# Optimization experiments

Measured on AMD Instinct MI355X. Metric: run time of the kernel, lower is better.

## Reference

```python
import jax, jax.numpy as jnp
import numpy as np
from jax import lax

B, T_HIST, T_PRED = 8192, 11, 80
IN, H = 2, 64


def _glorot(key, shape, fan):
    bound = 1.0 / np.sqrt(fan)
    return jax.random.uniform(key, shape, jnp.float32, -bound, bound)


def setup_inputs() -> dict:
    key = jax.random.key(0)
    ks = jax.random.split(key, 20)
    inp = {"x": jax.random.normal(ks[0], (B, T_HIST, IN), jnp.float32)}
    # encoder / decoder: 2-layer tanh RNN, PyTorch param layout (out_features first)
    for pfx, base in (("enc", 1), ("dec", 9)):
        inp[f"{pfx}_Wih0"] = _glorot(ks[base + 0], (H, IN), H)
        inp[f"{pfx}_Whh0"] = _glorot(ks[base + 1], (H, H), H)
        inp[f"{pfx}_bih0"] = _glorot(ks[base + 2], (H,), H)
        inp[f"{pfx}_bhh0"] = _glorot(ks[base + 3], (H,), H)
        inp[f"{pfx}_Wih1"] = _glorot(ks[base + 4], (H, H), H)
        inp[f"{pfx}_Whh1"] = _glorot(ks[base + 5], (H, H), H)
        inp[f"{pfx}_bih1"] = _glorot(ks[base + 6], (H,), H)
        inp[f"{pfx}_bhh1"] = _glorot(ks[base + 7], (H,), H)
    inp["fc_W"] = _glorot(ks[17], (2, H), H)
    inp["fc_b"] = _glorot(ks[18], (2,), H)
    return inp


def _rnn_layer(x_seq, h0, Wih, Whh, bih, bhh):
    # x_seq: [T, B, in]; tanh RNN cell, returns (h_T, all hidden states [T, B, H])
    def step(h, x_t):
        h_new = jnp.tanh(x_t @ Wih.T + bih + h @ Whh.T + bhh)
        return h_new, h_new
    return lax.scan(step, h0, x_seq)


def reference(x,
              enc_Wih0, enc_Whh0, enc_bih0, enc_bhh0,
              enc_Wih1, enc_Whh1, enc_bih1, enc_bhh1,
              dec_Wih0, dec_Whh0, dec_bih0, dec_bhh0,
              dec_Wih1, dec_Whh1, dec_bih1, dec_bhh1,
              fc_W, fc_b):
    b = x.shape[0]
    h0 = jnp.zeros((b, H), x.dtype)
    x_seq = jnp.swapaxes(x, 0, 1)  # [T, B, 2]
    # encoder (dropout inactive in eval)
    h1_T, hs0 = _rnn_layer(x_seq, h0, enc_Wih0, enc_Whh0, enc_bih0, enc_bhh0)
    h2_T, _ = _rnn_layer(hs0, h0, enc_Wih1, enc_Whh1, enc_bih1, enc_bhh1)

    def dec_step(carry, _):
        h1, h2, inp = carry
        h1 = jnp.tanh(inp @ dec_Wih0.T + dec_bih0 + h1 @ dec_Whh0.T + dec_bhh0)
        h2 = jnp.tanh(h1 @ dec_Wih1.T + dec_bih1 + h2 @ dec_Whh1.T + dec_bhh1)
        pred = h2 @ fc_W.T + fc_b  # [B, 2]
        return (h1, h2, pred), pred

    init = (h1_T, h2_T, x[:, -1, :])
    _, preds = lax.scan(dec_step, init, None, length=T_PRED)  # [80, B, 2]
    return jnp.swapaxes(preds, 0, 1)  # [B, 80, 2]
```

## Files before the change

kernel.cpp:

```cpp
#include <hip/hip_runtime.h>

typedef __attribute__((ext_vector_type(8))) __bf16 bf16x8;
typedef __attribute__((ext_vector_type(4))) float  f32x4;

namespace {
constexpr int kB    = 8192;
constexpr int kTH   = 11;
constexpr int kTP   = 80;
constexpr int kM    = 16;
constexpr int kStrH = 72;
}

union FragU { bf16x8 v; unsigned u[4]; };

__device__ __forceinline__ bf16x8 zero_frag() {
    FragU z; z.u[0] = z.u[1] = z.u[2] = z.u[3] = 0u; return z.v;
}

__device__ __forceinline__ unsigned pack_hi16(unsigned a, unsigned b) {
    return (a >> 16) | (b & 0xFFFF0000u);
}

__device__ __forceinline__ void split8(const float* f, bf16x8& hi, bf16x8& lo) {
    FragU H, L;
#pragma unroll
    for (int w = 0; w < 4; ++w) {
        const unsigned u0 = __float_as_uint(f[2 * w + 0]);
        const unsigned u1 = __float_as_uint(f[2 * w + 1]);
        const float h0 = __uint_as_float(u0 & 0xFFFF0000u);
        const float h1 = __uint_as_float(u1 & 0xFFFF0000u);
        const unsigned l0 = __float_as_uint(f[2 * w + 0] - h0);
        const unsigned l1 = __float_as_uint(f[2 * w + 1] - h1);
        H.u[w] = pack_hi16(u0, u1);
        L.u[w] = pack_hi16(l0, l1);
    }
    hi = H.v; lo = L.v;
}

__device__ __forceinline__ void loadB1(const float* __restrict__ W, int col, int q,
                                       bf16x8 (&Bh)[2], bf16x8 (&Bl)[2]) {
#pragma unroll
    for (int c = 0; c < 2; ++c) {
        const float* src = W + col * 64 + c * 32 + q * 8;
        const float4 a = reinterpret_cast<const float4*>(src)[0];
        const float4 b = reinterpret_cast<const float4*>(src)[1];
        float f[8] = {a.x, a.y, a.z, a.w, b.x, b.y, b.z, b.w};
        split8(f, Bh[c], Bl[c]);
    }
}

__device__ __forceinline__ void loadBfc(const float* __restrict__ fcW, int p, int q,
                                        bf16x8 (&Bh)[2], bf16x8 (&Bl)[2]) {
#pragma unroll
    for (int c = 0; c < 2; ++c) {
        float f[8];
#pragma unroll
        for (int j = 0; j < 8; ++j)
            f[j] = (p < 2) ? fcW[p * 64 + c * 32 + q * 8 + j] : 0.f;
        split8(f, Bh[c], Bl[c]);
    }
}

__device__ __forceinline__ void loadBG(const float* __restrict__ fcW, float w0, float w1,
                                       int q, bf16x8 (&Bh)[2], bf16x8 (&Bl)[2]) {
#pragma unroll
    for (int c = 0; c < 2; ++c) {
        float f[8];
#pragma unroll
        for (int j = 0; j < 8; ++j) {
            const int k = c * 32 + q * 8 + j;
            f[j] = w0 * fcW[k] + w1 * fcW[64 + k];
        }
        split8(f, Bh[c], Bl[c]);
    }
}

__device__ __forceinline__ void write_h(unsigned short* hi, unsigned short* lo,
                                        int idx, float h) {
    const unsigned u = __float_as_uint(h);
    hi[idx] = (unsigned short)(u >> 16);
    const float hf = __uint_as_float(u & 0xFFFF0000u);
    const float l  = h - hf;
    lo[idx] = (unsigned short)(__float_as_uint(l) >> 16);
}

__device__ __forceinline__ bf16x8 read_frag(const unsigned short* plane, int off) {
    return *reinterpret_cast<const bf16x8*>(plane + off);
}

__device__ __forceinline__ f32x4 mfma3(bf16x8 ah, bf16x8 al, bf16x8 bh, bf16x8 bl, f32x4 acc) {
    acc = __builtin_amdgcn_mfma_f32_16x16x32_bf16(ah, bh, acc, 0, 0, 0);
    acc = __builtin_amdgcn_mfma_f32_16x16x32_bf16(ah, bl, acc, 0, 0, 0);
    acc = __builtin_amdgcn_mfma_f32_16x16x32_bf16(al, bh, acc, 0, 0, 0);
    return acc;
}

__device__ __forceinline__ float fast_tanh(float x) {
    const float e = __builtin_amdgcn_exp2f(x * 2.8853900817779268f);
    return fmaf(-2.0f, __builtin_amdgcn_rcpf(e + 1.0f), 1.0f);
}

__global__ __attribute__((amdgpu_waves_per_eu(2, 2))) __launch_bounds__(256)
void traj_rnn_kernel(
    const float* __restrict__ x,
    const float* __restrict__ eWih0, const float* __restrict__ eWhh0,
    const float* __restrict__ ebih0, const float* __restrict__ ebhh0,
    const float* __restrict__ eWih1, const float* __restrict__ eWhh1,
    const float* __restrict__ ebih1, const float* __restrict__ ebhh1,
    const float* __restrict__ dWih0, const float* __restrict__ dWhh0,
    const float* __restrict__ dbih0, const float* __restrict__ dbhh0,
    const float* __restrict__ dWih1, const float* __restrict__ dWhh1,
    const float* __restrict__ dbih1, const float* __restrict__ dbhh1,
    const float* __restrict__ fcW, const float* __restrict__ fcb,
    float* __restrict__ out)
{
    const int tid  = threadIdx.x;
    const int wv   = tid >> 6;
    const int lane = tid & 63;
    const int p    = lane & 15;
    const int q    = lane >> 4;
    const int col  = wv * 16 + p;
    const int r0   = blockIdx.x * kM;

    __shared__ __align__(16) unsigned short Hhi1[kM * kStrH], Hlo1[kM * kStrH];
    __shared__ __align__(16) unsigned short Hhi2[kM * kStrH], Hlo2[kM * kStrH];
    __shared__ __align__(16) float xbuf[kM * kTH * 2];

    for (int i = tid; i < kM * kTH * 2; i += 256)
        xbuf[i] = x[r0 * (kTH * 2) + i];

    bf16x8 H1h[2], H1l[2], H2h[2], H2l[2];
#pragma unroll
    for (int c = 0; c < 2; ++c) {
        H1h[c] = zero_frag(); H1l[c] = zero_frag();
        H2h[c] = zero_frag(); H2l[c] = zero_frag();
    }
    __syncthreads();

    const int aoff = p * kStrH;

    {
        const float b0 = ebih0[col] + ebhh0[col];
        const float b1 = ebih1[col] + ebhh1[col];
        const float w0 = eWih0[col * 2 + 0];
        const float w1 = eWih0[col * 2 + 1];
        bf16x8 B0h[2], B0l[2], B1h[2], B1l[2], B2h[2], B2l[2];
        loadB1(eWhh0, col, q, B0h, B0l);
        loadB1(eWih1, col, q, B1h, B1l);
        loadB1(eWhh1, col, q, B2h, B2l);

        f32x4 P1 = {b0, b0, b0, b0};

#pragma unroll 1
        for (int t = 0; t < kTH; ++t) {
#pragma unroll
            for (int r = 0; r < 4; ++r) {
                const float2 xv = *reinterpret_cast<const float2*>(
                    &xbuf[(4 * q + r) * (kTH * 2) + 2 * t]);
                const float h1 = fast_tanh(fmaf(w0, xv.x, fmaf(w1, xv.y, P1[r])));
                write_h(Hhi1, Hlo1, (4 * q + r) * kStrH + col, h1);
            }
            f32x4 a2 = {b1, b1, b1, b1};
#pragma unroll
            for (int c = 0; c < 2; ++c)
                a2 = mfma3(H2h[c], H2l[c], B2h[c], B2l[c], a2);
            __syncthreads();

#pragma unroll
            for (int c = 0; c < 2; ++c) {
                H1h[c] = read_frag(Hhi1, aoff + c * 32 + q * 8);
                H1l[c] = read_frag(Hlo1, aoff + c * 32 + q * 8);
            }
#pragma unroll
            for (int c = 0; c < 2; ++c)
                a2 = mfma3(H1h[c], H1l[c], B1h[c], B1l[c], a2);
            f32x4 np = {b0, b0, b0, b0};
#pragma unroll
            for (int c = 0; c < 2; ++c)
                np = mfma3(H1h[c], H1l[c], B0h[c], B0l[c], np);
            P1 = np;

#pragma unroll
            for (int r = 0; r < 4; ++r) {
                const float h2 = fast_tanh(a2[r]);
                write_h(Hhi2, Hlo2, (4 * q + r) * kStrH + col, h2);
            }
            __syncthreads();
#pragma unroll
            for (int c = 0; c < 2; ++c) {
                H2h[c] = read_frag(Hhi2, aoff + c * 32 + q * 8);
                H2l[c] = read_frag(Hlo2, aoff + c * 32 + q * 8);
            }
        }
    }

    {
        const float b0 = dbih0[col] + dbhh0[col];
        const float b1 = dbih1[col] + dbhh1[col];
        const float w0 = dWih0[col * 2 + 0];
        const float w1 = dWih0[col * 2 + 1];
        const float fb0 = fcb[0];
        const float fb1 = fcb[1];
        const float b0p = b0 + w0 * fb0 + w1 * fb1;
        const float fbp = (p == 0) ? fb0 : fb1;
        bf16x8 B0h[2], B0l[2], B1h[2], B1l[2], B2h[2], B2l[2];
        bf16x8 BFh[2], BFl[2], BGh[2], BGl[2];
        loadB1(dWhh0, col, q, B0h, B0l);
        loadB1(dWih1, col, q, B1h, B1l);
        loadB1(dWhh1, col, q, B2h, B2l);
        loadBfc(fcW, p, q, BFh, BFl);
        loadBG(fcW, w0, w1, q, BGh, BGl);

        f32x4 P1 = {b0, b0, b0, b0};
#pragma unroll
        for (int c = 0; c < 2; ++c)
            P1 = mfma3(H1h[c], H1l[c], B0h[c], B0l[c], P1);
#pragma unroll
        for (int r = 0; r < 4; ++r) {
            const float2 xv = *reinterpret_cast<const float2*>(
                &xbuf[(4 * q + r) * (kTH * 2) + 2 * (kTH - 1)]);
            P1[r] = fmaf(w0, xv.x, fmaf(w1, xv.y, P1[r]));
        }

#pragma unroll 1
        for (int t = 0; t < kTP; ++t) {
#pragma unroll
            for (int r = 0; r < 4; ++r) {
                const float h1 = fast_tanh(P1[r]);
                write_h(Hhi1, Hlo1, (4 * q + r) * kStrH + col, h1);
            }
            f32x4 a2 = {b1, b1, b1, b1};
#pragma unroll
            for (int c = 0; c < 2; ++c)
                a2 = mfma3(H2h[c], H2l[c], B2h[c], B2l[c], a2);
            __syncthreads();

#pragma unroll
            for (int c = 0; c < 2; ++c) {
                H1h[c] = read_frag(Hhi1, aoff + c * 32 + q * 8);
                H1l[c] = read_frag(Hlo1, aoff + c * 32 + q * 8);
            }
#pragma unroll
            for (int c = 0; c < 2; ++c)
                a2 = mfma3(H1h[c], H1l[c], B1h[c], B1l[c], a2);
            f32x4 np = {b0p, b0p, b0p, b0p};
#pragma unroll
            for (int c = 0; c < 2; ++c)
                np = mfma3(H1h[c], H1l[c], B0h[c], B0l[c], np);

#pragma unroll
            for (int r = 0; r < 4; ++r) {
                const float h2 = fast_tanh(a2[r]);
                write_h(Hhi2, Hlo2, (4 * q + r) * kStrH + col, h2);
            }
            __syncthreads();

#pragma unroll
            for (int c = 0; c < 2; ++c) {
                H2h[c] = read_frag(Hhi2, aoff + c * 32 + q * 8);
                H2l[c] = read_frag(Hlo2, aoff + c * 32 + q * 8);
            }
#pragma unroll
            for (int c = 0; c < 2; ++c)
                np = mfma3(H2h[c], H2l[c], BGh[c], BGl[c], np);
            P1 = np;

            if (wv == 0) {
                f32x4 fcC = {0.f, 0.f, 0.f, 0.f};
#pragma unroll
                for (int c = 0; c < 2; ++c)
                    fcC = mfma3(H2h[c], H2l[c], BFh[c], BFl[c], fcC);
                if (p < 2) {
#pragma unroll
                    for (int r = 0; r < 4; ++r)
                        out[((r0 + 4 * q + r) * kTP + t) * 2 + p] = fcC[r] + fbp;
                }
            }
        }
    }
}

extern "C" void kernel_launch(void* const* d_in, const int* in_sizes, int n_in,
                              void* d_out, int out_size, void* d_ws, size_t ws_size,
                              hipStream_t stream) {
    const float* x     = (const float*)d_in[0];
    const float* eWih0 = (const float*)d_in[1];
    const float* eWhh0 = (const float*)d_in[2];
    const float* ebih0 = (const float*)d_in[3];
    const float* ebhh0 = (const float*)d_in[4];
    const float* eWih1 = (const float*)d_in[5];
    const float* eWhh1 = (const float*)d_in[6];
    const float* ebih1 = (const float*)d_in[7];
    const float* ebhh1 = (const float*)d_in[8];
    const float* dWih0 = (const float*)d_in[9];
    const float* dWhh0 = (const float*)d_in[10];
    const float* dbih0 = (const float*)d_in[11];
    const float* dbhh0 = (const float*)d_in[12];
    const float* dWih1 = (const float*)d_in[13];
    const float* dWhh1 = (const float*)d_in[14];
    const float* dbih1 = (const float*)d_in[15];
    const float* dbhh1 = (const float*)d_in[16];
    const float* fcW   = (const float*)d_in[17];
    const float* fcb   = (const float*)d_in[18];
    float* out = (float*)d_out;

    dim3 grid(kB / kM);
    dim3 block(256);
    traj_rnn_kernel<<<grid, block, 0, stream>>>(
        x, eWih0, eWhh0, ebih0, ebhh0, eWih1, eWhh1, ebih1, ebhh1,
        dWih0, dWhh0, dbih0, dbhh0, dWih1, dWhh1, dbih1, dbhh1,
        fcW, fcb, out);
}
```

Baseline: 172.2 us.

## Process two independent 16-row batch tiles per block to interleave recurrences

After: 201.6 us. 17.1% more time.

```diff
diff --git a/kernel.cpp b/kernel.cpp
--- a/kernel.cpp
+++ b/kernel.cpp
@@ -8,6 +8,7 @@
 constexpr int kTH   = 11;
 constexpr int kTP   = 80;
 constexpr int kM    = 16;
+constexpr int kT    = 2;
 constexpr int kStrH = 72;
 }
 
@@ -100,7 +101,7 @@
     return fmaf(-2.0f, __builtin_amdgcn_rcpf(e + 1.0f), 1.0f);
 }
 
-__global__ __attribute__((amdgpu_waves_per_eu(2, 2))) __launch_bounds__(256)
+__global__ __attribute__((amdgpu_waves_per_eu(1, 1))) __launch_bounds__(256)
 void traj_rnn_kernel(
     const float* __restrict__ x,
     const float* __restrict__ eWih0, const float* __restrict__ eWhh0,
@@ -120,21 +121,23 @@
     const int p    = lane & 15;
     const int q    = lane >> 4;
     const int col  = wv * 16 + p;
-    const int r0   = blockIdx.x * kM;
-
-    __shared__ __align__(16) unsigned short Hhi1[kM * kStrH], Hlo1[kM * kStrH];
-    __shared__ __align__(16) unsigned short Hhi2[kM * kStrH], Hlo2[kM * kStrH];
-    __shared__ __align__(16) float xbuf[kM * kTH * 2];
-
-    for (int i = tid; i < kM * kTH * 2; i += 256)
+    const int r0   = blockIdx.x * (kT * kM);
+
+    __shared__ __align__(16) unsigned short Hhi1[kT][kM * kStrH], Hlo1[kT][kM * kStrH];
+    __shared__ __align__(16) unsigned short Hhi2[kT][kM * kStrH], Hlo2[kT][kM * kStrH];
+    __shared__ __align__(16) float xbuf[kT * kM * kTH * 2];
+
+    for (int i = tid; i < kT * kM * kTH * 2; i += 256)
         xbuf[i] = x[r0 * (kTH * 2) + i];
 
-    bf16x8 H1h[2], H1l[2], H2h[2], H2l[2];
-#pragma unroll
-    for (int c = 0; c < 2; ++c) {
-        H1h[c] = zero_frag(); H1l[c] = zero_frag();
-        H2h[c] = zero_frag(); H2l[c] = zero_frag();
-    }
+    bf16x8 H1h[kT][2], H1l[kT][2], H2h[kT][2], H2l[kT][2];
+#pragma unroll
+    for (int u = 0; u < kT; ++u)
+#pragma unroll
+        for (int c = 0; c < 2; ++c) {
+            H1h[u][c] = zero_frag(); H1l[u][c] = zero_frag();
+            H2h[u][c] = zero_frag(); H2l[u][c] = zero_frag();
+        }
     __syncthreads();
 
     const int aoff = p * kStrH;
@@ -149,48 +152,62 @@
         loadB1(eWih1, col, q, B1h, B1l);
         loadB1(eWhh1, col, q, B2h, B2l);
 
-        f32x4 P1 = {b0, b0, b0, b0};
+        f32x4 P1[kT];
+#pragma unroll
+        for (int u = 0; u < kT; ++u) P1[u] = {b0, b0, b0, b0};
 
 #pragma unroll 1
         for (int t = 0; t < kTH; ++t) {
 #pragma unroll
-            for (int r = 0; r < 4; ++r) {
-                const float2 xv = *reinterpret_cast<const float2*>(
-                    &xbuf[(4 * q + r) * (kTH * 2) + 2 * t]);
-                const float h1 = fast_tanh(fmaf(w0, xv.x, fmaf(w1, xv.y, P1[r])));
-                write_h(Hhi1, Hlo1, (4 * q + r) * kStrH + col, h1);
-            }
-            f32x4 a2 = {b1, b1, b1, b1};
-#pragma unroll
-            for (int c = 0; c < 2; ++c)
-                a2 = mfma3(H2h[c], H2l[c], B2h[c], B2l[c], a2);
+            for (int u = 0; u < kT; ++u)
+#pragma unroll
+                for (int r = 0; r < 4; ++r) {
+                    const float2 xv = *reinterpret_cast<const float2*>(
+                        &xbuf[(u * kM + 4 * q + r) * (kTH * 2) + 2 * t]);
+                    const float h1 = fast_tanh(fmaf(w0, xv.x, fmaf(w1, xv.y, P1[u][r])));
+                    write_h(Hhi1[u], Hlo1[u], (4 * q + r) * kStrH + col, h1);
+                }
+            f32x4 a2[kT];
+#pragma unroll
+            for (int u = 0; u < kT; ++u) {
+                a2[u] = {b1, b1, b1, b1};
+#pragma unroll
+                for (int c = 0; c < 2; ++c)
+                    a2[u] = mfma3(H2h[u][c], H2l[u][c], B2h[c], B2l[c], a2[u]);
+            }
             __syncthreads();
 
 #pragma unroll
-            for (int c = 0; c < 2; ++c) {
-                H1h[c] = read_frag(Hhi1, aoff + c * 32 + q * 8);
-                H1l[c] = read_frag(Hlo1, aoff + c * 32 + q * 8);
-            }
-#pragma unroll
-            for (int c = 0; c < 2; ++c)
-                a2 = mfma3(H1h[c], H1l[c], B1h[c], B1l[c], a2);
-            f32x4 np = {b0, b0, b0, b0};
-#pragma unroll
-            for (int c = 0; c < 2; ++c)
-                np = mfma3(H1h[c], H1l[c], B0h[c], B0l[c], np);
-            P1 = np;
-
-#pragma unroll
-            for (int r = 0; r < 4; ++r) {
-                const float h2 = fast_tanh(a2[r]);
-                write_h(Hhi2, Hlo2, (4 * q + r) * kStrH + col, h2);
+            for (int u = 0; u < kT; ++u)
+#pragma unroll
+                for (int c = 0; c < 2; ++c) {
+                    H1h[u][c] = read_frag(Hhi1[u], aoff + c * 32 + q * 8);
+                    H1l[u][c] = read_frag(Hlo1[u], aoff + c * 32 + q * 8);
+                }
+#pragma unroll
+            for (int u = 0; u < kT; ++u) {
+#pragma unroll
+                for (int c = 0; c < 2; ++c)
+                    a2[u] = mfma3(H1h[u][c], H1l[u][c], B1h[c], B1l[c], a2[u]);
+                f32x4 np = {b0, b0, b0, b0};
+#pragma unroll
+                for (int c = 0; c < 2; ++c)
+                    np = mfma3(H1h[u][c], H1l[u][c], B0h[c], B0l[c], np);
+                P1[u] = np;
+#pragma unroll
+                for (int r = 0; r < 4; ++r) {
+                    const float h2 = fast_tanh(a2[u][r]);
+                    write_h(Hhi2[u], Hlo2[u], (4 * q + r) * kStrH + col, h2);
+                }
             }
             __syncthreads();
 #pragma unroll
-            for (int c = 0; c < 2; ++c) {
-                H2h[c] = read_frag(Hhi2, aoff + c * 32 + q * 8);
-                H2l[c] = read_frag(Hlo2, aoff + c * 32 + q * 8);
-            }
+            for (int u = 0; u < kT; ++u)
+#pragma unroll
+                for (int c = 0; c < 2; ++c) {
+                    H2h[u][c] = read_frag(Hhi2[u], aoff + c * 32 + q * 8);
+                    H2l[u][c] = read_frag(Hlo2[u], aoff + c * 32 + q * 8);
+                }
         }
     }
 
@@ -211,69 +228,93 @@
         loadBfc(fcW, p, q, BFh, BFl);
         loadBG(fcW, w0, w1, q, BGh, BGl);
 
-        f32x4 P1 = {b0, b0, b0, b0};
-#pragma unroll
-        for (int c = 0; c < 2; ++c)
-            P1 = mfma3(H1h[c], H1l[c], B0h[c], B0l[c], P1);
-#pragma unroll
-        for (int r = 0; r < 4; ++r) {
-            const float2 xv = *reinterpret_cast<const float2*>(
-                &xbuf[(4 * q + r) * (kTH * 2) + 2 * (kTH - 1)]);
-            P1[r] = fmaf(w0, xv.x, fmaf(w1, xv.y, P1[r]));
+        f32x4 P1[kT];
+#pragma unroll
+        for (int u = 0; u < kT; ++u) {
+            f32x4 a = {b0, b0, b0, b0};
+#pragma unroll
+            for (int c = 0; c < 2; ++c)
+                a = mfma3(H1h[u][c], H1l[u][c], B0h[c], B0l[c], a);
+#pragma unroll
+            for (int r = 0; r < 4; ++r) {
+                const float2 xv = *reinterpret_cast<const float2*>(
+                    &xbuf[(u * kM + 4 * q + r) * (kTH * 2) + 2 * (kTH - 1)]);
+                a[r] = fmaf(w0, xv.x, fmaf(w1, xv.y, a[r]));
+            }
+            P1[u] = a;
         }
 
 #pragma unroll 1
         for (int t = 0; t < kTP; ++t) {
 #pragma unroll
-            for (int r = 0; r < 4; ++r) {
-                const float h1 = fast_tanh(P1[r]);
-                write_h(Hhi1, Hlo1, (4 * q + r) * kStrH + col, h1);
-            }
-            f32x4 a2 = {b1, b1, b1, b1};
-#pragma unroll
-            for (int c = 0; c < 2; ++c)
-                a2 = mfma3(H2h[c], H2l[c], B2h[c], B2l[c], a2);
+            for (int u = 0; u < kT; ++u)
+#pragma unroll
+                for (int r = 0; r < 4; ++r) {
+                    const float h1 = fast_tanh(P1[u][r]);
+                    write_h(Hhi1[u], Hlo1[u], (4 * q + r) * kStrH + col, h1);
+                }
+            f32x4 a2[kT];
+#pragma unroll
+            for (int u = 0; u < kT; ++u) {
+                a2[u] = {b1, b1, b1, b1};
+#pragma unroll
+                for (int c = 0; c < 2; ++c)
+                    a2[u] = mfma3(H2h[u][c], H2l[u][c], B2h[c], B2l[c], a2[u]);
+            }
             __syncthreads();
 
 #pragma unroll
-            for (int c = 0; c < 2; ++c) {
-                H1h[c] = read_frag(Hhi1, aoff + c * 32 + q * 8);
-                H1l[c] = read_frag(Hlo1, aoff + c * 32 + q * 8);
-            }
-#pragma unroll
-            for (int c = 0; c < 2; ++c)
-                a2 = mfma3(H1h[c], H1l[c], B1h[c], B1l[c], a2);
-            f32x4 np = {b0p, b0p, b0p, b0p};
-#pragma unroll
-            for (int c = 0; c < 2; ++c)
-                np = mfma3(H1h[c], H1l[c], B0h[c], B0l[c], np);
-
-#pragma unroll
-            for (int r = 0; r < 4; ++r) {
-                const float h2 = fast_tanh(a2[r]);
-                write_h(Hhi2, Hlo2, (4 * q + r) * kStrH + col, h2);
+            for (int u = 0; u < kT; ++u)
+#pragma unroll
+                for (int c = 0; c < 2; ++c) {
+                    H1h[u][c] = read_frag(Hhi1[u], aoff + c * 32 + q * 8);
+                    H1l[u][c] = read_frag(Hlo1[u], aoff + c * 32 + q * 8);
+                }
+            f32x4 np[kT];
+#pragma unroll
+            for (int u = 0; u < kT; ++u) {
+#pragma unroll
+                for (int c = 0; c < 2; ++c)
+                    a2[u] = mfma3(H1h[u][c], H1l[u][c], B1h[c], B1l[c], a2[u]);
+                np[u] = {b0p, b0p, b0p, b0p};
+#pragma unroll
+                for (int c = 0; c < 2; ++c)
+                    np[u] = mfma3(H1h[u][c], H1l[u][c], B0h[c], B0l[c], np[u]);
+#pragma unroll
+                for (int r = 0; r < 4; ++r) {
+                    const float h2 = fast_tanh(a2[u][r]);
+                    write_h(Hhi2[u], Hlo2[u], (4 * q + r) * kStrH + col, h2);
+                }
             }
             __syncthreads();
 
 #pragma unroll
-            for (int c = 0; c < 2; ++c) {
-                H2h[c] = read_frag(Hhi2, aoff + c * 32 + q * 8);
-                H2l[c] = read_frag(Hlo2, aoff + c * 32 + q * 8);
-            }
-#pragma unroll
-            for (int c = 0; c < 2; ++c)
-                np = mfma3(H2h[c], H2l[c], BGh[c], BGl[c], np);
-            P1 = np;
+            for (int u = 0; u < kT; ++u)
+#pragma unroll
+                for (int c = 0; c < 2; ++c) {
+                    H2h[u][c] = read_frag(Hhi2[u], aoff + c * 32 + q * 8);
+                    H2l[u][c] = read_frag(Hlo2[u], aoff + c * 32 + q * 8);
+                }
+#pragma unroll
+            for (int u = 0; u < kT; ++u) {
+#pragma unroll
+                for (int c = 0; c < 2; ++c)
+                    np[u] = mfma3(H2h[u][c], H2l[u][c], BGh[c], BGl[c], np[u]);
+                P1[u] = np[u];
+            }
 
             if (wv == 0) {
-                f32x4 fcC = {0.f, 0.f, 0.f, 0.f};
-#pragma unroll
-                for (int c = 0; c < 2; ++c)
-                    fcC = mfma3(H2h[c], H2l[c], BFh[c], BFl[c], fcC);
-                if (p < 2) {
-#pragma unroll
-                    for (int r = 0; r < 4; ++r)
-                        out[((r0 + 4 * q + r) * kTP + t) * 2 + p] = fcC[r] + fbp;
+#pragma unroll
+                for (int u = 0; u < kT; ++u) {
+                    f32x4 fcC = {0.f, 0.f, 0.f, 0.f};
+#pragma unroll
+                    for (int c = 0; c < 2; ++c)
+                        fcC = mfma3(H2h[u][c], H2l[u][c], BFh[c], BFl[c], fcC);
+                    if (p < 2) {
+#pragma unroll
+                        for (int r = 0; r < 4; ++r)
+                            out[((r0 + u * kM + 4 * q + r) * kTP + t) * 2 + p] = fcC[r] + fbp;
+                    }
                 }
             }
         }
@@ -304,7 +345,7 @@
     const float* fcb   = (const float*)d_in[18];
     float* out = (float*)d_out;
 
-    dim3 grid(kB / kM);
+    dim3 grid(kB / (kT * kM));
     dim3 block(256);
     traj_rnn_kernel<<<grid, block, 0, stream>>>(
         x, eWih0, eWhh0, ebih0, ebhh0, eWih1, eWhh1, ebih1, ebhh1,
```
